# Kernel optimization log

Measured on AMD Instinct MI355X. Metric: run time of the kernel, lower is better.

Reference implementation:

```python
import jax, jax.numpy as jnp
import numpy as np

N_NODES = 100000
N_EDGES = 1600000
D_IN = 128
D_HID = 128
D_OUT = 1
N_GRAPHS = 64


def setup_inputs() -> dict:
    key = jax.random.key(0)
    ks = jax.random.split(key, 8)
    x = jax.random.normal(ks[0], (N_NODES, D_IN), dtype=jnp.float32)
    edge_index = jax.random.randint(ks[1], (2, N_EDGES), 0, N_NODES, dtype=jnp.int64)
    batch = jnp.sort(jax.random.randint(ks[2], (N_NODES,), 0, N_GRAPHS, dtype=jnp.int64))
    s1 = 1.0 / np.sqrt(D_IN)
    s2 = 1.0 / np.sqrt(D_HID)
    W1 = jax.random.normal(ks[3], (D_IN, D_HID), dtype=jnp.float32) * s1
    b1 = jnp.zeros((D_HID,), dtype=jnp.float32)
    W2 = jax.random.normal(ks[4], (D_HID, D_HID), dtype=jnp.float32) * s2
    b2 = jnp.zeros((D_HID,), dtype=jnp.float32)
    Wf = jax.random.normal(ks[5], (D_HID, D_OUT), dtype=jnp.float32) * s2
    bf = jnp.zeros((D_OUT,), dtype=jnp.float32)
    return {"x": x, "edge_index": edge_index, "batch": batch,
            "W1": W1, "b1": b1, "W2": W2, "b2": b2, "Wf": Wf, "bf": bf,
            "num_graphs": N_GRAPHS}


def reference(x, edge_index, batch, W1, b1, W2, b2, Wf, bf, num_graphs):
    n = x.shape[0]
    # GCNConv default: add self-loops, symmetric deg^{-1/2} normalization
    loop = jnp.arange(n, dtype=edge_index.dtype)
    src = jnp.concatenate([edge_index[0], loop])  # [E+N]
    dst = jnp.concatenate([edge_index[1], loop])
    deg = jax.ops.segment_sum(jnp.ones(src.shape, x.dtype), dst, num_segments=n)
    dinv = jnp.where(deg > 0, jax.lax.rsqrt(jnp.maximum(deg, 1.0)), 0.0)
    norm = dinv[src] * dinv[dst]  # [E+N]

    def gcn_conv(h, W, b):
        h = h @ W  # [N, d_out] linear first (GCNConv fuses lin before propagate)
        msg = h[src] * norm[:, None]  # gather + scale
        return jax.ops.segment_sum(msg, dst, num_segments=n) + b  # scatter-add

    h = jax.nn.relu(gcn_conv(x, W1, b1))
    h = jax.nn.relu(gcn_conv(h, W2, b2))

    # global_mean_pool over batch assignment
    gsum = jax.ops.segment_sum(h, batch, num_segments=num_graphs)
    cnt = jax.ops.segment_sum(jnp.ones((n,), x.dtype), batch, num_segments=num_graphs)
    pooled = gsum / jnp.maximum(cnt, 1.0)[:, None]  # [G, d_hid]

    return (pooled @ Wf + bf).squeeze(-1)  # [G]
```

## Files before the change

kernel.cpp:

```cpp
#include <hip/hip_runtime.h>
#include <hip/hip_bf16.h>
#include <math.h>


#define DFEAT 128
#define SCAN_NB 256
#define SCAN_TPB 256
#define FILL_CHUNKS 256

typedef unsigned int uint32;
typedef __attribute__((ext_vector_type(8))) short bf16x8;
typedef __attribute__((ext_vector_type(4))) float f32x4;

__device__ __forceinline__ uint32 f2bf_rne(float f) {
    uint32 x = __float_as_uint(f);
    return (x + 0x7fffu + ((x >> 16) & 1u)) >> 16;
}
__device__ __forceinline__ uint32 packbf2(float lo, float hi) {
    return f2bf_rne(lo) | (f2bf_rne(hi) << 16);
}
__device__ __forceinline__ float bflo(uint32 u) { return __uint_as_float(u << 16); }
__device__ __forceinline__ float bfhi(uint32 u) { return __uint_as_float(u & 0xffff0000u); }

__global__ void k_zero2(int* __restrict__ a, int* __restrict__ b, int n) {
    int i = blockIdx.x * blockDim.x + threadIdx.x;
    if (i < n) { a[i] = 0; b[i] = 0; }
}

__global__ void k_zero_f(float* __restrict__ p, int n) {
    int i = blockIdx.x * blockDim.x + threadIdx.x;
    if (i < n) p[i] = 0.f;
}

__global__ void k_degcount(const int* __restrict__ dst, int* __restrict__ degcnt, int E) {
    int e = blockIdx.x * blockDim.x + threadIdx.x;
    if (e < E) atomicAdd(&degcnt[dst[e]], 1);
}

__global__ __launch_bounds__(256) void k_wt(const float* __restrict__ W,
                                            unsigned short* __restrict__ Wt) {
    int idx = blockIdx.x * 256 + threadIdx.x;
    if (idx < 128 * 128) {
        int n = idx >> 7, k = idx & 127;
        Wt[idx] = (unsigned short)f2bf_rne(W[(k << 7) + n]);
    }
}

__global__ __launch_bounds__(SCAN_TPB) void k_partsum(const int* __restrict__ deg,
                                                      int* __restrict__ bsum,
                                                      int N, int chunk) {
    int b = blockIdx.x, tid = threadIdx.x;
    int beg = b * chunk, end = min(N, beg + chunk);
    int s = 0;
    for (int i = beg + tid; i < end; i += SCAN_TPB) s += deg[i];
    __shared__ int lds[SCAN_TPB];
    lds[tid] = s;
    __syncthreads();
    for (int off = SCAN_TPB / 2; off > 0; off >>= 1) {
        if (tid < off) lds[tid] += lds[tid + off];
        __syncthreads();
    }
    if (tid == 0) bsum[b] = lds[0];
}

__global__ __launch_bounds__(SCAN_NB) void k_scanb(int* __restrict__ bsum) {
    __shared__ int lds[SCAN_NB];
    int tid = threadIdx.x;
    int v = bsum[tid];
    lds[tid] = v;
    __syncthreads();
    for (int off = 1; off < SCAN_NB; off <<= 1) {
        int t = (tid >= off) ? lds[tid - off] : 0;
        __syncthreads();
        lds[tid] += t;
        __syncthreads();
    }
    bsum[tid] = lds[tid] - v;
}

__global__ __launch_bounds__(SCAN_TPB) void k_writeptr(const int* __restrict__ deg,
                                                       const int* __restrict__ bbase,
                                                       int* __restrict__ rowptr,
                                                       float* __restrict__ dinv,
                                                       int N, int chunk) {
    int b = blockIdx.x, tid = threadIdx.x;
    int beg = b * chunk, end = min(N, beg + chunk);
    int per = (chunk + SCAN_TPB - 1) / SCAN_TPB;
    int tbeg = beg + tid * per;
    int tend = min(end, tbeg + per);
    int s = 0;
    for (int i = tbeg; i < tend; ++i) s += deg[i];
    __shared__ int lds[SCAN_TPB];
    lds[tid] = s;
    __syncthreads();
    for (int off = 1; off < SCAN_TPB; off <<= 1) {
        int t = (tid >= off) ? lds[tid - off] : 0;
        __syncthreads();
        lds[tid] += t;
        __syncthreads();
    }
    int run = bbase[b] + ((tid == 0) ? 0 : lds[tid - 1]);
    for (int i = tbeg; i < tend; ++i) {
        int d = deg[i];
        rowptr[i] = run;
        dinv[i] = rsqrtf((float)(d + 1));
        run += d;
    }
    if (tend == N && tbeg < tend) rowptr[N] = run;
}

__global__ __launch_bounds__(256) void k_fill(const int* __restrict__ src,
                                              const int* __restrict__ dst,
                                              const int* __restrict__ rowptr,
                                              int* __restrict__ fill,
                                              int* __restrict__ col, int E) {
    int r = blockIdx.x & 7;
    int chunk = blockIdx.x >> 3;
    int per = (E + FILL_CHUNKS - 1) / FILL_CHUNKS;
    int beg = chunk * per;
    int end = min(E, beg + per);
    int e = beg + threadIdx.x;
    for (; e + 768 < end; e += 1024) {
        int d0 = __builtin_nontemporal_load(&dst[e +   0]);
        int d1 = __builtin_nontemporal_load(&dst[e + 256]);
        int d2 = __builtin_nontemporal_load(&dst[e + 512]);
        int d3 = __builtin_nontemporal_load(&dst[e + 768]);
        int s0 = __builtin_nontemporal_load(&src[e +   0]);
        int s1 = __builtin_nontemporal_load(&src[e + 256]);
        int s2 = __builtin_nontemporal_load(&src[e + 512]);
        int s3 = __builtin_nontemporal_load(&src[e + 768]);
        if (((d0 >> 9) & 7) == r) { int p = rowptr[d0] + atomicAdd(&fill[d0], 1); col[p] = s0; }
        if (((d1 >> 9) & 7) == r) { int p = rowptr[d1] + atomicAdd(&fill[d1], 1); col[p] = s1; }
        if (((d2 >> 9) & 7) == r) { int p = rowptr[d2] + atomicAdd(&fill[d2], 1); col[p] = s2; }
        if (((d3 >> 9) & 7) == r) { int p = rowptr[d3] + atomicAdd(&fill[d3], 1); col[p] = s3; }
    }
    for (; e < end; e += 256) {
        int d = __builtin_nontemporal_load(&dst[e]);
        if (((d >> 9) & 7) == r) {
            int s = __builtin_nontemporal_load(&src[e]);
            int pos = rowptr[d] + atomicAdd(&fill[d], 1);
            col[pos] = s;
        }
    }
}

__global__ __launch_bounds__(256, 3) void k_linear_mfma(const float* __restrict__ H,
                                                        const uint32* __restrict__ Wt,
                                                        uint32* __restrict__ C,
                                                        int N, int ntiles) {
    __shared__ uint32 WtS[128 * 64];
    __shared__ uint32 inS[64 * 64];
    int tid = threadIdx.x;
    int lane = tid & 63;
    int wv = tid >> 6;
    int g = lane >> 4;
    int r = lane & 15;
    int swz = (r & 7) << 4;
    {
        const uint4* srcp = (const uint4*)Wt;
#pragma unroll
        for (int i = 0; i < 8; ++i) {
            int c = tid + i * 256;
            int n = c >> 4, off = c & 15;
            int b = (n * 256 + off * 16) ^ ((n & 7) << 4);
            *(uint4*)((char*)WtS + b) = srcp[c];
        }
    }
    for (int t = blockIdx.x; t < ntiles; t += gridDim.x) {
        int rbase = t << 6;
        __syncthreads();
        {
            const float4* H4 = (const float4*)(H + (size_t)rbase * DFEAT);
            int limrow = N - rbase;
#pragma unroll
            for (int i = 0; i < 4; ++i) {
                int c = tid + i * 256;
                int m = c >> 4, off = c & 15;
                uint4 w2 = make_uint4(0u, 0u, 0u, 0u);
                if (m < limrow) {
                    float4 f0 = H4[m * 32 + off * 2];
                    float4 f1 = H4[m * 32 + off * 2 + 1];
                    w2.x = packbf2(f0.x, f0.y); w2.y = packbf2(f0.z, f0.w);
                    w2.z = packbf2(f1.x, f1.y); w2.w = packbf2(f1.z, f1.w);
                }
                int b = (m * 256 + off * 16) ^ ((m & 7) << 4);
                *(uint4*)((char*)inS + b) = w2;
            }
        }
        __syncthreads();
        f32x4 acc[8];
#pragma unroll
        for (int nt = 0; nt < 8; ++nt) acc[nt] = (f32x4){0.f, 0.f, 0.f, 0.f};
        int mrow = wv * 16 + r;
        const char* inB = (const char*)inS + mrow * 256;
#pragma unroll
        for (int kk = 0; kk < 4; ++kk) {
            int koff = (kk * 64 + g * 16) ^ swz;
            bf16x8 bfrag = *(const bf16x8*)(inB + koff);
#pragma unroll
            for (int nt = 0; nt < 8; ++nt) {
                bf16x8 afrag = *(const bf16x8*)((const char*)WtS + (nt * 16 + r) * 256 + koff);
                acc[nt] = __builtin_amdgcn_mfma_f32_16x16x32_bf16(afrag, bfrag, acc[nt], 0, 0, 0);
            }
        }
        int m = rbase + mrow;
        if (m < N) {
            uint2* Crow = (uint2*)(C + (size_t)m * 64);
#pragma unroll
            for (int nt = 0; nt < 8; ++nt) {
                uint2 u;
                u.x = packbf2(acc[nt].x, acc[nt].y);
                u.y = packbf2(acc[nt].z, acc[nt].w);
                Crow[nt * 4 + g] = u;
            }
        }
    }
}

__global__ __launch_bounds__(256) void k_agg(const uint32* __restrict__ Tb,
                                             float2* __restrict__ Hout,
                                             const int* __restrict__ col,
                                             const int* __restrict__ rowptr,
                                             const float* __restrict__ dinv,
                                             const float* __restrict__ bias, int N) {
    int lane = threadIdx.x & 63;
    int node = blockIdx.x * 4 + (threadIdx.x >> 6);
    if (node >= N) return;
    float2 b = ((const float2*)bias)[lane];
    float di = dinv[node];
    uint32 us = Tb[(size_t)node * 64 + lane];
    float ws = di * di;
    float2 acc;
    acc.x = bflo(us) * ws;
    acc.y = bfhi(us) * ws;
    int beg = rowptr[node], end = rowptr[node + 1];
    int j = beg;
    for (; j + 3 < end; j += 4) {
        int s0 = col[j + 0];
        int s1 = col[j + 1];
        int s2 = col[j + 2];
        int s3 = col[j + 3];
        float w0 = dinv[s0] * di;
        float w1 = dinv[s1] * di;
        float w2 = dinv[s2] * di;
        float w3 = dinv[s3] * di;
        uint32 u0 = Tb[(size_t)s0 * 64 + lane];
        uint32 u1 = Tb[(size_t)s1 * 64 + lane];
        uint32 u2 = Tb[(size_t)s2 * 64 + lane];
        uint32 u3 = Tb[(size_t)s3 * 64 + lane];
        acc.x += w0 * bflo(u0); acc.y += w0 * bfhi(u0);
        acc.x += w1 * bflo(u1); acc.y += w1 * bfhi(u1);
        acc.x += w2 * bflo(u2); acc.y += w2 * bfhi(u2);
        acc.x += w3 * bflo(u3); acc.y += w3 * bfhi(u3);
    }
    for (; j < end; ++j) {
        int s = col[j];
        float w = dinv[s] * di;
        uint32 u = Tb[(size_t)s * 64 + lane];
        acc.x += w * bflo(u);
        acc.y += w * bfhi(u);
    }
    acc.x = fmaxf(acc.x + b.x, 0.f);
    acc.y = fmaxf(acc.y + b.y, 0.f);
    Hout[(size_t)node * 64 + lane] = acc;
}

__global__ __launch_bounds__(256) void k_pool_sum(const float2* __restrict__ Hn,
                                                  const int* __restrict__ batch,
                                                  float* __restrict__ gsum,
                                                  int N, int waves_total) {
    int w = blockIdx.x * 4 + (threadIdx.x >> 6);
    int lane = threadIdx.x & 63;
    int per = (N + waves_total - 1) / waves_total;
    int n0 = w * per;
    int n1 = min(N, n0 + per);
    if (n0 >= n1) return;
    int gcur = batch[n0];
    float2 acc = make_float2(0.f, 0.f);
    for (int i = n0; i < n1; ++i) {
        int g = batch[i];
        if (g != gcur) {
            atomicAdd(&gsum[gcur * DFEAT + lane * 2 + 0], acc.x);
            atomicAdd(&gsum[gcur * DFEAT + lane * 2 + 1], acc.y);
            acc = make_float2(0.f, 0.f);
            gcur = g;
        }
        float2 v = Hn[(size_t)i * 64 + lane];
        acc.x += v.x;
        acc.y += v.y;
    }
    atomicAdd(&gsum[gcur * DFEAT + lane * 2 + 0], acc.x);
    atomicAdd(&gsum[gcur * DFEAT + lane * 2 + 1], acc.y);
}

__global__ __launch_bounds__(128) void k_head(const float* __restrict__ gsum,
                                              const int* __restrict__ batch,
                                              const float* __restrict__ Wf,
                                              const float* __restrict__ bf,
                                              float* __restrict__ out, int N) {
    int g = blockIdx.x;
    int tid = threadIdx.x;
    int l = 0, h = N;
    while (l < h) { int m = (l + h) >> 1; if (batch[m] < g) l = m + 1; else h = m; }
    int lo = l;
    h = N;
    while (l < h) { int m = (l + h) >> 1; if (batch[m] < g + 1) l = m + 1; else h = m; }
    int hi = l;
    float cnt = (float)((hi - lo) > 0 ? (hi - lo) : 1);
    float val = (gsum[g * DFEAT + tid] / cnt) * Wf[tid];
    for (int off = 32; off >= 1; off >>= 1) val += __shfl_down(val, off, 64);
    __shared__ float ws2[2];
    if ((tid & 63) == 0) ws2[tid >> 6] = val;
    __syncthreads();
    if (tid == 0) out[g] = ws2[0] + ws2[1] + bf[0];
}

extern "C" void kernel_launch(void* const* d_in, const int* in_sizes, int n_in,
                              void* d_out, int out_size, void* d_ws, size_t ws_size,
                              hipStream_t stream) {
    const float* x    = (const float*)d_in[0];
    const int*   ei   = (const int*)d_in[1];
    const int*   batch= (const int*)d_in[2];
    const float* W1   = (const float*)d_in[3];
    const float* b1   = (const float*)d_in[4];
    const float* W2   = (const float*)d_in[5];
    const float* b2   = (const float*)d_in[6];
    const float* Wf   = (const float*)d_in[7];
    const float* bf   = (const float*)d_in[8];

    int N = in_sizes[0] / DFEAT;
    int E = in_sizes[1] / 2;
    int G = out_size;

    const int* src = ei;
    const int* dst = ei + E;

    char* wsb = (char*)d_ws;
    size_t off = 0;
    auto walloc = [&](size_t bytes) {
        void* p = wsb + off;
        off = (off + bytes + 255) & ~(size_t)255;
        return p;
    };
    uint32* A     = (uint32*)walloc((size_t)N * 64 * sizeof(uint32));
    float* B      = (float*)walloc((size_t)N * DFEAT * sizeof(float));
    float* dinv   = (float*)walloc((size_t)N * sizeof(float));
    int*   rowptr = (int*)  walloc((size_t)(N + 1) * sizeof(int));
    int*   col    = (int*)  walloc((size_t)E * sizeof(int));
    int*   degcnt = (int*)  walloc((size_t)N * sizeof(int));
    int*   fill   = (int*)  walloc((size_t)N * sizeof(int));
    float* gsum   = (float*)walloc((size_t)G * DFEAT * sizeof(float));
    int*   bsum   = (int*)  walloc((size_t)SCAN_NB * sizeof(int));
    unsigned short* Wt1 = (unsigned short*)walloc(128 * 128 * sizeof(unsigned short));
    unsigned short* Wt2 = (unsigned short*)walloc(128 * 128 * sizeof(unsigned short));
    (void)ws_size; (void)n_in;

    int gN = (N + 255) / 256;
    int gE = (E + 255) / 256;
    int chunk = (N + SCAN_NB - 1) / SCAN_NB;
    int ntiles = (N + 63) >> 6;

    k_zero2<<<gN, 256, 0, stream>>>(degcnt, fill, N);
    k_zero_f<<<(G * DFEAT + 255) / 256, 256, 0, stream>>>(gsum, G * DFEAT);
    k_wt<<<64, 256, 0, stream>>>(W1, Wt1);
    k_wt<<<64, 256, 0, stream>>>(W2, Wt2);
    k_degcount<<<gE, 256, 0, stream>>>(dst, degcnt, E);
    k_partsum<<<SCAN_NB, SCAN_TPB, 0, stream>>>(degcnt, bsum, N, chunk);
    k_scanb<<<1, SCAN_NB, 0, stream>>>(bsum);
    k_writeptr<<<SCAN_NB, SCAN_TPB, 0, stream>>>(degcnt, bsum, rowptr, dinv, N, chunk);
    k_fill<<<FILL_CHUNKS * 8, 256, 0, stream>>>(src, dst, rowptr, fill, col, E);

    k_linear_mfma<<<768, 256, 0, stream>>>(x, (const uint32*)Wt1, A, N, ntiles);
    k_agg<<<(N + 3) / 4, 256, 0, stream>>>(A, (float2*)B, col, rowptr, dinv, b1, N);
    k_linear_mfma<<<768, 256, 0, stream>>>(B, (const uint32*)Wt2, A, N, ntiles);
    k_agg<<<(N + 3) / 4, 256, 0, stream>>>(A, (float2*)B, col, rowptr, dinv, b2, N);

    const int POOL_BLOCKS = 1024;
    k_pool_sum<<<POOL_BLOCKS, 256, 0, stream>>>((const float2*)B, batch, gsum, N, POOL_BLOCKS * 4);
    k_head<<<G, 128, 0, stream>>>(gsum, batch, Wf, bf, (float*)d_out, N);
}
```

Before: 380.0 us.

## Route degree-count and CSR-fill atomics to XCC-local partitions via ticket work stealing

The degree-count and CSR fill kernels now read the hardware XCC id and use global ticket counters, so each block first takes chunks of the edge list for the node partition tied to its own XCC, then steals other partitions' chunks. The goal is to keep atomics on degcnt/fill for a given node range inside one XCC's L2, cutting cross-die coherence traffic. The ticket counters are zeroed together with gsum by extending that zero kernel. In exchange, every edge chunk is read eight times in degcount (once per partition), the nontemporal loads and 4-way unrolling in fill are dropped, and each chunk grab costs a global atomic plus two barriers.

```diff
diff --git a/kernel.cpp b/kernel.cpp
--- a/kernel.cpp
+++ b/kernel.cpp
@@ -22,6 +22,12 @@
 __device__ __forceinline__ float bflo(uint32 u) { return __uint_as_float(u << 16); }
 __device__ __forceinline__ float bfhi(uint32 u) { return __uint_as_float(u & 0xffff0000u); }
 
+__device__ __forceinline__ int xcc_id() {
+    int x;
+    asm volatile("s_getreg_b32 %0, hwreg(HW_REG_XCC_ID)" : "=s"(x));
+    return x & 7;
+}
+
 __global__ void k_zero2(int* __restrict__ a, int* __restrict__ b, int n) {
     int i = blockIdx.x * blockDim.x + threadIdx.x;
     if (i < n) { a[i] = 0; b[i] = 0; }
@@ -32,9 +38,27 @@
     if (i < n) p[i] = 0.f;
 }
 
-__global__ void k_degcount(const int* __restrict__ dst, int* __restrict__ degcnt, int E) {
-    int e = blockIdx.x * blockDim.x + threadIdx.x;
-    if (e < E) atomicAdd(&degcnt[dst[e]], 1);
+__global__ __launch_bounds__(256) void k_degcount(const int* __restrict__ dst,
+                                                  int* __restrict__ degcnt,
+                                                  int* __restrict__ tickets, int E) {
+    int myr = xcc_id();
+    int per = (E + FILL_CHUNKS - 1) / FILL_CHUNKS;
+    __shared__ int chunkS;
+    for (int rr = 0; rr < 8; ++rr) {
+        int role = (myr + rr) & 7;
+        for (;;) {
+            if (threadIdx.x == 0) chunkS = atomicAdd(&tickets[role], 1);
+            __syncthreads();
+            int c = chunkS;
+            __syncthreads();
+            if (c >= FILL_CHUNKS) break;
+            int beg = c * per, end = min(E, beg + per);
+            for (int e = beg + threadIdx.x; e < end; e += 256) {
+                int d = dst[e];
+                if (((d >> 9) & 7) == role) atomicAdd(&degcnt[d], 1);
+            }
+        }
+    }
 }
 
 __global__ __launch_bounds__(256) void k_wt(const float* __restrict__ W,
@@ -113,33 +137,27 @@
                                               const int* __restrict__ dst,
                                               const int* __restrict__ rowptr,
                                               int* __restrict__ fill,
-                                              int* __restrict__ col, int E) {
-    int r = blockIdx.x & 7;
-    int chunk = blockIdx.x >> 3;
+                                              int* __restrict__ col,
+                                              int* __restrict__ tickets, int E) {
+    int myr = xcc_id();
     int per = (E + FILL_CHUNKS - 1) / FILL_CHUNKS;
-    int beg = chunk * per;
-    int end = min(E, beg + per);
-    int e = beg + threadIdx.x;
-    for (; e + 768 < end; e += 1024) {
-        int d0 = __builtin_nontemporal_load(&dst[e +   0]);
-        int d1 = __builtin_nontemporal_load(&dst[e + 256]);
-        int d2 = __builtin_nontemporal_load(&dst[e + 512]);
-        int d3 = __builtin_nontemporal_load(&dst[e + 768]);
-        int s0 = __builtin_nontemporal_load(&src[e +   0]);
-        int s1 = __builtin_nontemporal_load(&src[e + 256]);
-        int s2 = __builtin_nontemporal_load(&src[e + 512]);
-        int s3 = __builtin_nontemporal_load(&src[e + 768]);
-        if (((d0 >> 9) & 7) == r) { int p = rowptr[d0] + atomicAdd(&fill[d0], 1); col[p] = s0; }
-        if (((d1 >> 9) & 7) == r) { int p = rowptr[d1] + atomicAdd(&fill[d1], 1); col[p] = s1; }
-        if (((d2 >> 9) & 7) == r) { int p = rowptr[d2] + atomicAdd(&fill[d2], 1); col[p] = s2; }
-        if (((d3 >> 9) & 7) == r) { int p = rowptr[d3] + atomicAdd(&fill[d3], 1); col[p] = s3; }
-    }
-    for (; e < end; e += 256) {
-        int d = __builtin_nontemporal_load(&dst[e]);
-        if (((d >> 9) & 7) == r) {
-            int s = __builtin_nontemporal_load(&src[e]);
-            int pos = rowptr[d] + atomicAdd(&fill[d], 1);
-            col[pos] = s;
+    __shared__ int chunkS;
+    for (int rr = 0; rr < 8; ++rr) {
+        int role = (myr + rr) & 7;
+        for (;;) {
+            if (threadIdx.x == 0) chunkS = atomicAdd(&tickets[role], 1);
+            __syncthreads();
+            int c = chunkS;
+            __syncthreads();
+            if (c >= FILL_CHUNKS) break;
+            int beg = c * per, end = min(E, beg + per);
+            for (int e = beg + threadIdx.x; e < end; e += 256) {
+                int d = dst[e];
+                if (((d >> 9) & 7) == role) {
+                    int pos = rowptr[d] + atomicAdd(&fill[d], 1);
+                    col[pos] = src[e];
+                }
+            }
         }
     }
 }
@@ -350,25 +368,25 @@
     int*   degcnt = (int*)  walloc((size_t)N * sizeof(int));
     int*   fill   = (int*)  walloc((size_t)N * sizeof(int));
     float* gsum   = (float*)walloc((size_t)G * DFEAT * sizeof(float));
+    int*   tickets= (int*)  walloc(16 * sizeof(int));
     int*   bsum   = (int*)  walloc((size_t)SCAN_NB * sizeof(int));
     unsigned short* Wt1 = (unsigned short*)walloc(128 * 128 * sizeof(unsigned short));
     unsigned short* Wt2 = (unsigned short*)walloc(128 * 128 * sizeof(unsigned short));
     (void)ws_size; (void)n_in;
 
     int gN = (N + 255) / 256;
-    int gE = (E + 255) / 256;
     int chunk = (N + SCAN_NB - 1) / SCAN_NB;
     int ntiles = (N + 63) >> 6;
 
     k_zero2<<<gN, 256, 0, stream>>>(degcnt, fill, N);
-    k_zero_f<<<(G * DFEAT + 255) / 256, 256, 0, stream>>>(gsum, G * DFEAT);
+    k_zero_f<<<(G * DFEAT + 16 + 255) / 256, 256, 0, stream>>>(gsum, G * DFEAT + 16);
     k_wt<<<64, 256, 0, stream>>>(W1, Wt1);
     k_wt<<<64, 256, 0, stream>>>(W2, Wt2);
-    k_degcount<<<gE, 256, 0, stream>>>(dst, degcnt, E);
+    k_degcount<<<2048, 256, 0, stream>>>(dst, degcnt, tickets, E);
     k_partsum<<<SCAN_NB, SCAN_TPB, 0, stream>>>(degcnt, bsum, N, chunk);
     k_scanb<<<1, SCAN_NB, 0, stream>>>(bsum);
     k_writeptr<<<SCAN_NB, SCAN_TPB, 0, stream>>>(degcnt, bsum, rowptr, dinv, N, chunk);
-    k_fill<<<FILL_CHUNKS * 8, 256, 0, stream>>>(src, dst, rowptr, fill, col, E);
+    k_fill<<<2048, 256, 0, stream>>>(src, dst, rowptr, fill, col, tickets + 8, E);
 
     k_linear_mfma<<<768, 256, 0, stream>>>(x, (const uint32*)Wt1, A, N, ntiles);
     k_agg<<<(N + 3) / 4, 256, 0, stream>>>(A, (float2*)B, col, rowptr, dinv, b1, N);
```

Result: slower. 768.1 us (+102.1%).
